# Kernel optimization log

Hardware: AMD Instinct MI355X
Metric: run time of the kernel (lower is better)

## Reference

```python
import jax, jax.numpy as jnp
import numpy as np


def setup_inputs() -> dict:
    key = jax.random.key(0)
    ks = jax.random.split(key, 6)
    B, T, D, N = 8, 4096, 1024, 16
    s = 0.02  # small init scale for linear weights
    return {
        "x": jax.random.normal(ks[0], (B, T, D), jnp.float32),
        "Wd": jax.random.normal(ks[1], (D, D), jnp.float32) * s,
        "bd": jnp.zeros((D,), jnp.float32),
        "Wb": jax.random.normal(ks[2], (D, N), jnp.float32) * s,
        "bb": jnp.zeros((N,), jnp.float32),
        "Wc": jax.random.normal(ks[3], (D, N), jnp.float32) * s,
        "bc": jnp.zeros((N,), jnp.float32),
        "Wo": jax.random.normal(ks[4], (D, D), jnp.float32) * s,
        "bo": jnp.zeros((D,), jnp.float32),
        "A": jax.random.normal(ks[5], (D, N), jnp.float32) * 0.01,
    }


def reference(x, Wd, bd, Wb, bb, Wc, bc, Wo, bo, A):
    # x: (B, T, D). All per-step projections are time-independent -> batch them.
    delta = jax.nn.softplus(x @ Wd + bd)              # (B, T, D)
    dbar = jnp.mean(delta, axis=-1, keepdims=True)    # (B, T, 1) scalar gate per step
    Bt = x @ Wb + bb                                  # (B, T, N)
    Ct = x @ Wc + bc                                  # (B, T, N)
    sA = jax.nn.sigmoid(jnp.mean(A, axis=0))          # (N,)

    a = 1.0 - dbar                                    # (B, T, 1) decay
    b = dbar * Bt * sA                                # (B, T, N) input injection

    def step(h, ab):
        at, bt = ab                                   # at: (B,1), bt: (B,N)
        h = h * at + bt
        return h, h

    h0 = jnp.zeros((x.shape[0], A.shape[1]), x.dtype)
    # scan over time axis (leading)
    _, hs = jax.lax.scan(step, h0, (jnp.swapaxes(a, 0, 1), jnp.swapaxes(b, 0, 1)))
    hs = jnp.swapaxes(hs, 0, 1)                       # (B, T, N)

    y = jnp.sum(hs * Ct, axis=-1, keepdims=True) * x  # (B, T, D); (h*C).sum expanded * x
    return y @ Wo + bo
```

## Files before the change

kernel.cpp:

```cpp
#include <hip/hip_runtime.h>
#include <hip/hip_bf16.h>


typedef __bf16 bfx4 __attribute__((ext_vector_type(4)));
typedef __bf16 bfx8 __attribute__((ext_vector_type(8)));
typedef float  f32x4 __attribute__((ext_vector_type(4)));

#define M_ROWS 32768
#define DDIM   1024
#define NSTATE 16
#define TLEN   4096
#define BATCH  8
#define CHUNK  32
#define NCHUNK 128
#define NGROUP (BATCH * NCHUNK)

#define BK     32
#define KT     (DDIM / BK)
#define TILEE  16384

__global__ __launch_bounds__(256) void transpose_w_kernel(
    const float* __restrict__ Wd, const float* __restrict__ Wo,
    __bf16* __restrict__ WdT, __bf16* __restrict__ WoT)
{
    __shared__ float tile[32][33];
    const int bid = blockIdx.x;
    const float* src = (bid < 1024) ? Wd : Wo;
    __bf16* dst = (bid < 1024) ? WdT : WoT;
    const int t = bid & 1023;
    const int tr = t >> 5, tc = t & 31;
    const int tx = threadIdx.x & 31, ty = threadIdx.x >> 5;
#pragma unroll
    for (int i = 0; i < 4; ++i) {
        int r = ty + i * 8;
        tile[r][tx] = src[(size_t)(tr * 32 + r) * 1024 + tc * 32 + tx];
    }
    __syncthreads();
#pragma unroll
    for (int i = 0; i < 4; ++i) {
        int r = ty + i * 8;
        dst[(size_t)(tc * 32 + r) * 1024 + tr * 32 + tx] = (__bf16)tile[tx][r];
    }
}

__global__ __launch_bounds__(256) void wbc_kernel(
    const float* __restrict__ Wb, const float* __restrict__ Wc,
    __bf16* __restrict__ Wbc)
{
    int idx = blockIdx.x * 256 + threadIdx.x;
    int n2 = idx >> 10, k = idx & 1023;
    float v = (n2 < 16) ? Wb[k * 16 + n2] : Wc[k * 16 + (n2 - 16)];
    Wbc[idx] = (__bf16)v;
}

__global__ __launch_bounds__(256) void sA_kernel(const float* __restrict__ A,
                                                 float* __restrict__ sA)
{
    __shared__ float red[256];
    int tid = threadIdx.x;
    int n = tid & 15, part = tid >> 4;
    float sum = 0.f;
    for (int k = part * 64; k < part * 64 + 64; ++k) sum += A[k * 16 + n];
    red[tid] = sum;
    __syncthreads();
    if (tid < 16) {
        float tot = 0.f;
        for (int p = 0; p < 16; ++p) tot += red[p * 16 + tid];
        sA[tid] = 1.f / (1.f + expf(-tot * (1.f / 1024.f)));
    }
}

__global__ __launch_bounds__(256) void cast_kernel(const float* __restrict__ x,
                                                   __bf16* __restrict__ xb)
{
    size_t i = ((size_t)blockIdx.x * 256 + threadIdx.x) * 8;
    const float4* xg = (const float4*)(x + i);
    float4 v0 = xg[0], v1 = xg[1];
    bfx8 o;
    o[0] = (__bf16)v0.x; o[1] = (__bf16)v0.y; o[2] = (__bf16)v0.z; o[3] = (__bf16)v0.w;
    o[4] = (__bf16)v1.x; o[5] = (__bf16)v1.y; o[6] = (__bf16)v1.z; o[7] = (__bf16)v1.w;
    *(bfx8*)(xb + i) = o;
}

__global__ __launch_bounds__(256) void btct_kernel(
    const __bf16* __restrict__ xb, const __bf16* __restrict__ Wbc,
    const float* __restrict__ bb, const float* __restrict__ bc,
    float* __restrict__ Bt, float* __restrict__ Ct)
{
    const int wid = blockIdx.x * 4 + (threadIdx.x >> 6);
    const int lane = threadIdx.x & 63;
    const int quad = lane >> 4, l15 = lane & 15;
    const int mbase = wid * 16;
    const __bf16* ga = xb + (size_t)(mbase + l15) * 1024 + quad * 8;
    const __bf16* gb = Wbc + (size_t)l15 * 1024 + quad * 8;
    const __bf16* gc = Wbc + (size_t)(16 + l15) * 1024 + quad * 8;
    f32x4 accB = {0.f, 0.f, 0.f, 0.f};
    f32x4 accC = {0.f, 0.f, 0.f, 0.f};
#pragma unroll 4
    for (int k = 0; k < 1024; k += 32) {
        bfx8 a = *(const bfx8*)ga;  ga += 32;
        bfx8 b = *(const bfx8*)gb;  gb += 32;
        bfx8 c = *(const bfx8*)gc;  gc += 32;
        accB = __builtin_amdgcn_mfma_f32_16x16x32_bf16(a, b, accB, 0, 0, 0);
        accC = __builtin_amdgcn_mfma_f32_16x16x32_bf16(a, c, accC, 0, 0, 0);
    }
#pragma unroll
    for (int r = 0; r < 4; ++r) {
        int row = mbase + quad * 4 + r;
        Bt[row * 16 + l15] = accB[r] + bb[l15];
        Ct[row * 16 + l15] = accC[r] + bc[l15];
    }
}

__device__ __forceinline__ void gload16(const void* g, void* l)
{
    __builtin_amdgcn_global_load_lds((__attribute__((address_space(1))) void*)g,
                                     (__attribute__((address_space(3))) void*)l,
                                     16, 0, 0);
}

__device__ __forceinline__ void tile_swizzle256(int L, int& mtile, int& ntile)
{
    int xcd = L & 7;
    int s = L >> 3;
    mtile = xcd * 16 + (s >> 2);
    ntile = s & 3;
}

__device__ __forceinline__ void stage_tile(const __bf16* pA0, const __bf16* pA1,
                                           const __bf16* pB0, const __bf16* pB1,
                                           __bf16* lbase, int tid, int t)
{
    const size_t ko = (size_t)t * BK;
    __bf16* ba = lbase;
    __bf16* bb2 = lbase + 8192;
    gload16(pA0 + ko, ba + tid * 8);
    gload16(pA1 + ko, ba + 4096 + tid * 8);
    gload16(pB0 + ko, bb2 + tid * 8);
    gload16(pB1 + ko, bb2 + 4096 + tid * 8);
}

__device__ __forceinline__ void gemm_core256(const __bf16* __restrict__ Abuf,
                                             const __bf16* __restrict__ Bbuf,
                                             __bf16* lds,
                                             int mbase, int nbase,
                                             f32x4 acc[8][4])
{
    const int tid = threadIdx.x;
    const int lane = tid & 63;
    const int w = tid >> 6;
    const int quad = lane >> 4, l15 = lane & 15;
    const int wm = w >> 2, wn = w & 3;

    const int row0 = ((tid >> 6) << 4) + ((tid >> 2) & 15);
    const int kc   = (tid & 3) ^ ((tid >> 3) & 3);
    const __bf16* pA0 = Abuf + (size_t)(mbase + row0) * DDIM + kc * 8;
    const __bf16* pA1 = pA0 + (size_t)128 * DDIM;
    const __bf16* pB0 = Bbuf + (size_t)(nbase + row0) * DDIM + kc * 8;
    const __bf16* pB1 = pB0 + (size_t)128 * DDIM;

    const int vsw  = l15 * 4 + (quad ^ ((l15 >> 1) & 3));
    const int aoff = wm * 8 * 512 + vsw * 8;
    const int boff = wn * 4 * 512 + vsw * 8;

    stage_tile(pA0, pA1, pB0, pB1, lds + 0 * TILEE, tid, 0);
    stage_tile(pA0, pA1, pB0, pB1, lds + 1 * TILEE, tid, 1);
    stage_tile(pA0, pA1, pB0, pB1, lds + 2 * TILEE, tid, 2);

#pragma unroll 1
    for (int t = 0; t < KT; ++t) {
        if (t < KT - 2)       asm volatile("s_waitcnt vmcnt(8)" ::: "memory");
        else if (t == KT - 2) asm volatile("s_waitcnt vmcnt(4)" ::: "memory");
        else                  asm volatile("s_waitcnt vmcnt(0)" ::: "memory");
        __builtin_amdgcn_s_barrier();
        __builtin_amdgcn_sched_barrier(0);

        const __bf16* Al = lds + (t & 3) * TILEE;
        const __bf16* Bl = Al + 8192;
        const size_t ko3 = (size_t)(t + 3) * BK;
        __bf16* lb3 = lds + ((t + 3) & 3) * TILEE;

        bfx8 bfr[4], af[4], ag[4];
#pragma unroll
        for (int j = 0; j < 4; ++j) bfr[j] = *(const bfx8*)(Bl + boff + j * 512);
#pragma unroll
        for (int i = 0; i < 4; ++i) af[i]  = *(const bfx8*)(Al + aoff + i * 512);
        if (t < KT - 3) {
            gload16(pA0 + ko3, lb3 + tid * 8);
            gload16(pA1 + ko3, lb3 + 4096 + tid * 8);
        }
#pragma unroll
        for (int i = 0; i < 4; ++i) ag[i] = *(const bfx8*)(Al + aoff + (4 + i) * 512);
        if (t < KT - 3) {
            gload16(pB0 + ko3, lb3 + 8192 + tid * 8);
            gload16(pB1 + ko3, lb3 + 8192 + 4096 + tid * 8);
        }
        asm volatile("s_waitcnt lgkmcnt(4)" ::: "memory");
        __builtin_amdgcn_sched_barrier(0);
        __builtin_amdgcn_s_setprio(1);
#pragma unroll
        for (int i = 0; i < 4; ++i)
#pragma unroll
            for (int j = 0; j < 4; ++j)
                acc[i][j] = __builtin_amdgcn_mfma_f32_16x16x32_bf16(
                    af[i], bfr[j], acc[i][j], 0, 0, 0);
        __builtin_amdgcn_s_setprio(0);
        asm volatile("s_waitcnt lgkmcnt(0)" ::: "memory");
        __builtin_amdgcn_sched_barrier(0);
        __builtin_amdgcn_s_setprio(1);
#pragma unroll
        for (int i = 0; i < 4; ++i)
#pragma unroll
            for (int j = 0; j < 4; ++j)
                acc[4 + i][j] = __builtin_amdgcn_mfma_f32_16x16x32_bf16(
                    ag[i], bfr[j], acc[4 + i][j], 0, 0, 0);
        __builtin_amdgcn_s_setprio(0);
    }
}

__global__ __launch_bounds__(512, 2) void gemm1_kernel(
    const __bf16* __restrict__ xb, const __bf16* __restrict__ WdT,
    const float* __restrict__ bd, float* __restrict__ dbar)
{
    __shared__ __bf16 lds[4 * TILEE];
    f32x4 acc[8][4];
    f32x4 z4 = {0.f, 0.f, 0.f, 0.f};
#pragma unroll
    for (int i = 0; i < 8; ++i)
#pragma unroll
        for (int j = 0; j < 4; ++j) acc[i][j] = z4;

    int mtile, ntile;
    tile_swizzle256(blockIdx.x, mtile, ntile);
    const int mbase = mtile * 256;
    const int nbase = ntile * 256;
    gemm_core256(xb, WdT, lds, mbase, nbase, acc);

    const int lane = threadIdx.x & 63;
    const int w = threadIdx.x >> 6;
    const int quad = lane >> 4, l15 = lane & 15;
    const int wm = w >> 2, wn = w & 3;
    const float invD = 1.0f / 1024.0f;
#pragma unroll
    for (int i = 0; i < 8; ++i) {
#pragma unroll
        for (int r = 0; r < 4; ++r) {
            float sp = 0.f;
#pragma unroll
            for (int j = 0; j < 4; ++j) {
                int col = nbase + wn * 64 + j * 16 + l15;
                float z = acc[i][j][r] + bd[col];
                sp += fmaxf(z, 0.f) + __logf(1.f + __expf(-fabsf(z)));
            }
#pragma unroll
            for (int off = 1; off < 16; off <<= 1) sp += __shfl_xor(sp, off, 16);
            if (l15 == 0) {
                int row = mbase + wm * 128 + i * 16 + quad * 4 + r;
                atomicAdd(&dbar[row], sp * invD);
            }
        }
    }
}

__global__ __launch_bounds__(512, 2) void gemm2_kernel(
    const __bf16* __restrict__ xb, const __bf16* __restrict__ WoT,
    const float* __restrict__ srow, const float* __restrict__ bo,
    float* __restrict__ out)
{
    __shared__ __bf16 lds[4 * TILEE];
    f32x4 acc[8][4];
    f32x4 z4 = {0.f, 0.f, 0.f, 0.f};
#pragma unroll
    for (int i = 0; i < 8; ++i)
#pragma unroll
        for (int j = 0; j < 4; ++j) acc[i][j] = z4;

    int mtile, ntile;
    tile_swizzle256(blockIdx.x, mtile, ntile);
    const int mbase = mtile * 256;
    const int nbase = ntile * 256;
    gemm_core256(xb, WoT, lds, mbase, nbase, acc);

    const int lane = threadIdx.x & 63;
    const int w = threadIdx.x >> 6;
    const int quad = lane >> 4, l15 = lane & 15;
    const int wm = w >> 2, wn = w & 3;
#pragma unroll
    for (int i = 0; i < 8; ++i) {
        int row0 = mbase + wm * 128 + i * 16 + quad * 4;
#pragma unroll
        for (int r = 0; r < 4; ++r) {
            float sv = srow[row0 + r];
#pragma unroll
            for (int j = 0; j < 4; ++j) {
                int col = nbase + wn * 64 + j * 16 + l15;
                out[(size_t)(row0 + r) * 1024 + col] = sv * acc[i][j][r] + bo[col];
            }
        }
    }
}

__global__ __launch_bounds__(256) void scan_kernel(
    const float* __restrict__ dbar, const float* __restrict__ Bt,
    const float* __restrict__ Ct, const float* __restrict__ sA,
    float* __restrict__ s_local, float* __restrict__ pbuf,
    float* __restrict__ Pc, float* __restrict__ Hend)
{
    int tid = threadIdx.x;
    int gid = blockIdx.x * 16 + (tid >> 4);
    int n = tid & 15;
    int b = gid >> 7;
    int c = gid & 127;
    float sAn = sA[n];
    float h = 0.f, p = 1.f;
    int row = b * TLEN + c * CHUNK;
#pragma unroll 4
    for (int t = 0; t < CHUNK; ++t, ++row) {
        float d = dbar[row];
        float btv = Bt[row * 16 + n];
        float ctv = Ct[row * 16 + n];
        float a = 1.f - d;
        h = h * a + d * sAn * btv;
        p *= a;
        float prod = h * ctv;
#pragma unroll
        for (int off = 1; off < 16; off <<= 1) prod += __shfl_xor(prod, off, 16);
        if (n == 0) { s_local[row] = prod; pbuf[row] = p; }
    }
    Hend[gid * 16 + n] = h;
    if (n == 0) Pc[gid] = p;
}

__global__ __launch_bounds__(128) void stitch_kernel(
    const float* __restrict__ Pc, const float* __restrict__ Hend,
    float* __restrict__ h0buf)
{
    int tid = threadIdx.x;
    int b = tid >> 4, n = tid & 15;
    float h0 = 0.f;
#pragma unroll 8
    for (int c = 0; c < NCHUNK; ++c) {
        int g = b * NCHUNK + c;
        h0buf[g * 16 + n] = h0;
        h0 = Pc[g] * h0 + Hend[g * 16 + n];
    }
}

__global__ __launch_bounds__(256) void fixup_kernel(
    const float* __restrict__ s_local, const float* __restrict__ pbuf,
    const float* __restrict__ h0buf, const float* __restrict__ Ct,
    float* __restrict__ sbuf)
{
    int row = blockIdx.x * 256 + threadIdx.x;
    int b = row >> 12, t = row & 4095;
    int g = b * NCHUNK + (t / CHUNK);
    const float4* h4 = (const float4*)(h0buf + g * 16);
    const float4* c4 = (const float4*)(Ct + (size_t)row * 16);
    float dot = 0.f;
#pragma unroll
    for (int q = 0; q < 4; ++q) {
        float4 hv = h4[q], cv = c4[q];
        dot += hv.x * cv.x + hv.y * cv.y + hv.z * cv.z + hv.w * cv.w;
    }
    sbuf[row] = s_local[row] + pbuf[row] * dot;
}

extern "C" void kernel_launch(void* const* d_in, const int* in_sizes, int n_in,
                              void* d_out, int out_size, void* d_ws, size_t ws_size,
                              hipStream_t stream)
{
    const float* x  = (const float*)d_in[0];
    const float* Wd = (const float*)d_in[1];
    const float* bd = (const float*)d_in[2];
    const float* Wb = (const float*)d_in[3];
    const float* bb = (const float*)d_in[4];
    const float* Wc = (const float*)d_in[5];
    const float* bc = (const float*)d_in[6];
    const float* Wo = (const float*)d_in[7];
    const float* bo = (const float*)d_in[8];
    const float* A  = (const float*)d_in[9];
    float* out = (float*)d_out;

    char* base = (char*)d_ws;
    size_t off = 0;
    auto alloc = [&](size_t bytes) -> void* {
        void* p = base + off;
        off = (off + bytes + 255) & ~(size_t)255;
        return p;
    };
    __bf16* xb   = (__bf16*)alloc((size_t)M_ROWS * DDIM * 2);
    __bf16* WdT  = (__bf16*)alloc((size_t)DDIM * DDIM * 2);
    __bf16* WoT  = (__bf16*)alloc((size_t)DDIM * DDIM * 2);
    __bf16* Wbc  = (__bf16*)alloc(32 * 1024 * 2);
    float* sAbuf = (float*)alloc(64);
    float* dbar  = (float*)alloc(M_ROWS * 4);
    float* Bt    = (float*)alloc((size_t)M_ROWS * 16 * 4);
    float* Ct    = (float*)alloc((size_t)M_ROWS * 16 * 4);
    float* s_loc = (float*)alloc(M_ROWS * 4);
    float* pbuf  = (float*)alloc(M_ROWS * 4);
    float* sbuf  = (float*)alloc(M_ROWS * 4);
    float* Pc    = (float*)alloc(NGROUP * 4);
    float* Hend  = (float*)alloc(NGROUP * 16 * 4);
    float* h0buf = (float*)alloc(NGROUP * 16 * 4);

    transpose_w_kernel<<<2048, 256, 0, stream>>>(Wd, Wo, WdT, WoT);
    wbc_kernel<<<128, 256, 0, stream>>>(Wb, Wc, Wbc);
    sA_kernel<<<1, 256, 0, stream>>>(A, sAbuf);
    cast_kernel<<<M_ROWS * DDIM / 8 / 256, 256, 0, stream>>>(x, xb);
    (void)hipMemsetAsync(dbar, 0, M_ROWS * 4, stream);
    btct_kernel<<<512, 256, 0, stream>>>(xb, Wbc, bb, bc, Bt, Ct);
    gemm1_kernel<<<512, 512, 0, stream>>>(xb, WdT, bd, dbar);
    scan_kernel<<<NGROUP / 16, 256, 0, stream>>>(dbar, Bt, Ct, sAbuf, s_loc, pbuf, Pc, Hend);
    stitch_kernel<<<1, 128, 0, stream>>>(Pc, Hend, h0buf);
    fixup_kernel<<<M_ROWS / 256, 256, 0, stream>>>(s_loc, pbuf, h0buf, Ct, sbuf);
    gemm2_kernel<<<512, 512, 0, stream>>>(xb, WoT, sbuf, bo, out);
}
```

Before: 461.2 us.

## Fuse prep kernels into one launch and fold stitch into fixup

Merges the weight transpose, Wb/Wc packing, sA reduction, x cast and dbar zeroing into a single block-dispatched prep kernel, replacing four launches and a memset. Removes the single-block stitch kernel by having each fixup block recompute its chunk-start states serially over prior chunks into shared memory. This cuts launch overhead and a serial single-block step, but adds redundant sequential work per fixup block (up to 128 chunk steps on 16 threads).

After: 458.7 us. No clear change (-0.5%).

```diff
diff --git a/kernel.cpp b/kernel.cpp
--- a/kernel.cpp
+++ b/kernel.cpp
@@ -19,67 +19,73 @@
 #define KT     (DDIM / BK)
 #define TILEE  16384
 
-__global__ __launch_bounds__(256) void transpose_w_kernel(
+#define NB_TR   2048
+#define NB_WBC  128
+#define B_SA    (NB_TR + NB_WBC)
+#define B_CAST  (B_SA + 1)
+#define NB_CAST (M_ROWS * DDIM / 8 / 256)
+#define B_ZERO  (B_CAST + NB_CAST)
+#define NB_ZERO (M_ROWS / 256)
+#define NB_PREP (B_ZERO + NB_ZERO)
+
+__global__ __launch_bounds__(256) void prep_kernel(
     const float* __restrict__ Wd, const float* __restrict__ Wo,
-    __bf16* __restrict__ WdT, __bf16* __restrict__ WoT)
+    const float* __restrict__ Wb, const float* __restrict__ Wc,
+    const float* __restrict__ A,  const float* __restrict__ x,
+    __bf16* __restrict__ WdT, __bf16* __restrict__ WoT,
+    __bf16* __restrict__ Wbc, float* __restrict__ sA,
+    __bf16* __restrict__ xb,  float* __restrict__ dbar)
 {
     __shared__ float tile[32][33];
     const int bid = blockIdx.x;
-    const float* src = (bid < 1024) ? Wd : Wo;
-    __bf16* dst = (bid < 1024) ? WdT : WoT;
-    const int t = bid & 1023;
-    const int tr = t >> 5, tc = t & 31;
-    const int tx = threadIdx.x & 31, ty = threadIdx.x >> 5;
-#pragma unroll
-    for (int i = 0; i < 4; ++i) {
-        int r = ty + i * 8;
-        tile[r][tx] = src[(size_t)(tr * 32 + r) * 1024 + tc * 32 + tx];
-    }
-    __syncthreads();
-#pragma unroll
-    for (int i = 0; i < 4; ++i) {
-        int r = ty + i * 8;
-        dst[(size_t)(tc * 32 + r) * 1024 + tr * 32 + tx] = (__bf16)tile[tx][r];
-    }
-}
-
-__global__ __launch_bounds__(256) void wbc_kernel(
-    const float* __restrict__ Wb, const float* __restrict__ Wc,
-    __bf16* __restrict__ Wbc)
-{
-    int idx = blockIdx.x * 256 + threadIdx.x;
-    int n2 = idx >> 10, k = idx & 1023;
-    float v = (n2 < 16) ? Wb[k * 16 + n2] : Wc[k * 16 + (n2 - 16)];
-    Wbc[idx] = (__bf16)v;
-}
-
-__global__ __launch_bounds__(256) void sA_kernel(const float* __restrict__ A,
-                                                 float* __restrict__ sA)
-{
-    __shared__ float red[256];
-    int tid = threadIdx.x;
-    int n = tid & 15, part = tid >> 4;
-    float sum = 0.f;
-    for (int k = part * 64; k < part * 64 + 64; ++k) sum += A[k * 16 + n];
-    red[tid] = sum;
-    __syncthreads();
-    if (tid < 16) {
-        float tot = 0.f;
-        for (int p = 0; p < 16; ++p) tot += red[p * 16 + tid];
-        sA[tid] = 1.f / (1.f + expf(-tot * (1.f / 1024.f)));
-    }
-}
-
-__global__ __launch_bounds__(256) void cast_kernel(const float* __restrict__ x,
-                                                   __bf16* __restrict__ xb)
-{
-    size_t i = ((size_t)blockIdx.x * 256 + threadIdx.x) * 8;
-    const float4* xg = (const float4*)(x + i);
-    float4 v0 = xg[0], v1 = xg[1];
-    bfx8 o;
-    o[0] = (__bf16)v0.x; o[1] = (__bf16)v0.y; o[2] = (__bf16)v0.z; o[3] = (__bf16)v0.w;
-    o[4] = (__bf16)v1.x; o[5] = (__bf16)v1.y; o[6] = (__bf16)v1.z; o[7] = (__bf16)v1.w;
-    *(bfx8*)(xb + i) = o;
+    const int tid = threadIdx.x;
+
+    if (bid < NB_TR) {
+        const float* src = (bid < 1024) ? Wd : Wo;
+        __bf16* dst = (bid < 1024) ? WdT : WoT;
+        const int t = bid & 1023;
+        const int tr = t >> 5, tc = t & 31;
+        const int tx = tid & 31, ty = tid >> 5;
+#pragma unroll
+        for (int i = 0; i < 4; ++i) {
+            int r = ty + i * 8;
+            tile[r][tx] = src[(size_t)(tr * 32 + r) * 1024 + tc * 32 + tx];
+        }
+        __syncthreads();
+#pragma unroll
+        for (int i = 0; i < 4; ++i) {
+            int r = ty + i * 8;
+            dst[(size_t)(tc * 32 + r) * 1024 + tr * 32 + tx] = (__bf16)tile[tx][r];
+        }
+    } else if (bid < B_SA) {
+        int idx = (bid - NB_TR) * 256 + tid;
+        int n2 = idx >> 10, k = idx & 1023;
+        float v = (n2 < 16) ? Wb[k * 16 + n2] : Wc[k * 16 + (n2 - 16)];
+        Wbc[idx] = (__bf16)v;
+    } else if (bid == B_SA) {
+        __shared__ float red[256];
+        int n = tid & 15, part = tid >> 4;
+        float sum = 0.f;
+        for (int k = part * 64; k < part * 64 + 64; ++k) sum += A[k * 16 + n];
+        red[tid] = sum;
+        __syncthreads();
+        if (tid < 16) {
+            float tot = 0.f;
+            for (int p = 0; p < 16; ++p) tot += red[p * 16 + tid];
+            sA[tid] = 1.f / (1.f + expf(-tot * (1.f / 1024.f)));
+        }
+    } else if (bid < B_ZERO) {
+        size_t i = ((size_t)(bid - B_CAST) * 256 + tid) * 8;
+        const float4* xg = (const float4*)(x + i);
+        float4 v0 = xg[0], v1 = xg[1];
+        bfx8 o;
+        o[0] = (__bf16)v0.x; o[1] = (__bf16)v0.y; o[2] = (__bf16)v0.z; o[3] = (__bf16)v0.w;
+        o[4] = (__bf16)v1.x; o[5] = (__bf16)v1.y; o[6] = (__bf16)v1.z; o[7] = (__bf16)v1.w;
+        *(bfx8*)(xb + i) = o;
+    } else {
+        int row = (bid - B_ZERO) * 256 + tid;
+        dbar[row] = 0.f;
+    }
 }
 
 __global__ __launch_bounds__(256) void btct_kernel(
@@ -331,30 +337,30 @@
     if (n == 0) Pc[gid] = p;
 }
 
-__global__ __launch_bounds__(128) void stitch_kernel(
-    const float* __restrict__ Pc, const float* __restrict__ Hend,
-    float* __restrict__ h0buf)
-{
-    int tid = threadIdx.x;
-    int b = tid >> 4, n = tid & 15;
-    float h0 = 0.f;
-#pragma unroll 8
-    for (int c = 0; c < NCHUNK; ++c) {
-        int g = b * NCHUNK + c;
-        h0buf[g * 16 + n] = h0;
-        h0 = Pc[g] * h0 + Hend[g * 16 + n];
-    }
-}
-
 __global__ __launch_bounds__(256) void fixup_kernel(
     const float* __restrict__ s_local, const float* __restrict__ pbuf,
-    const float* __restrict__ h0buf, const float* __restrict__ Ct,
-    float* __restrict__ sbuf)
-{
-    int row = blockIdx.x * 256 + threadIdx.x;
-    int b = row >> 12, t = row & 4095;
-    int g = b * NCHUNK + (t / CHUNK);
-    const float4* h4 = (const float4*)(h0buf + g * 16);
+    const float* __restrict__ Pc, const float* __restrict__ Hend,
+    const float* __restrict__ Ct, float* __restrict__ sbuf)
+{
+    __shared__ float H0_s[8][16];
+    const int tid = threadIdx.x;
+    const int row0 = blockIdx.x * 256;
+    const int b = row0 >> 12;
+    const int cstart = (row0 & 4095) >> 5;
+    if (tid < 16) {
+        float h0 = 0.f;
+        const int gbase = b * NCHUNK;
+        const int cend = cstart + 8;
+#pragma unroll 8
+        for (int c = 0; c < cend; ++c) {
+            if (c >= cstart) H0_s[c - cstart][tid] = h0;
+            h0 = Pc[gbase + c] * h0 + Hend[(gbase + c) * 16 + tid];
+        }
+    }
+    __syncthreads();
+    const int row = row0 + tid;
+    const int lc = (tid >> 5);
+    const float4* h4 = (const float4*)(&H0_s[lc][0]);
     const float4* c4 = (const float4*)(Ct + (size_t)row * 16);
     float dot = 0.f;
 #pragma unroll
@@ -401,17 +407,12 @@
     float* sbuf  = (float*)alloc(M_ROWS * 4);
     float* Pc    = (float*)alloc(NGROUP * 4);
     float* Hend  = (float*)alloc(NGROUP * 16 * 4);
-    float* h0buf = (float*)alloc(NGROUP * 16 * 4);
-
-    transpose_w_kernel<<<2048, 256, 0, stream>>>(Wd, Wo, WdT, WoT);
-    wbc_kernel<<<128, 256, 0, stream>>>(Wb, Wc, Wbc);
-    sA_kernel<<<1, 256, 0, stream>>>(A, sAbuf);
-    cast_kernel<<<M_ROWS * DDIM / 8 / 256, 256, 0, stream>>>(x, xb);
-    (void)hipMemsetAsync(dbar, 0, M_ROWS * 4, stream);
+
+    prep_kernel<<<NB_PREP, 256, 0, stream>>>(Wd, Wo, Wb, Wc, A, x,
+                                             WdT, WoT, Wbc, sAbuf, xb, dbar);
     btct_kernel<<<512, 256, 0, stream>>>(xb, Wbc, bb, bc, Bt, Ct);
     gemm1_kernel<<<512, 512, 0, stream>>>(xb, WdT, bd, dbar);
     scan_kernel<<<NGROUP / 16, 256, 0, stream>>>(dbar, Bt, Ct, sAbuf, s_loc, pbuf, Pc, Hend);
-    stitch_kernel<<<1, 128, 0, stream>>>(Pc, Hend, h0buf);
-    fixup_kernel<<<M_ROWS / 256, 256, 0, stream>>>(s_loc, pbuf, h0buf, Ct, sbuf);
+    fixup_kernel<<<M_ROWS / 256, 256, 0, stream>>>(s_loc, pbuf, Pc, Hend, Ct, sbuf);
     gemm2_kernel<<<512, 512, 0, stream>>>(xb, WoT, sbuf, bo, out);
 }
```
